# Performance work log

Measured on AMD Instinct MI355X. Metric: run time of the kernel, lower is better.

The kernel has to match this reference:

```python
import jax, jax.numpy as jnp
import numpy as np
import math


def _conv1x1(x, w):
    # x: [B,C,H,W], w: [O,I,1,1] (OIHW)
    return jax.lax.conv_general_dilated(x, w, (1, 1), 'VALID',
                                        dimension_numbers=('NCHW', 'OIHW', 'NCHW'))


def _dwconv3x3(x, w):
    # depthwise 3x3, padding=1; w: [C,1,3,3]
    return jax.lax.conv_general_dilated(x, w, (1, 1), 'SAME',
                                        dimension_numbers=('NCHW', 'OIHW', 'NCHW'),
                                        feature_group_count=x.shape[1])


def setup_inputs() -> dict:
    key = jax.random.key(0)
    ks = jax.random.split(key, 8)
    B, H, W, C = 4, 1024, 1024, 3
    s = 0.3
    return {
        'x': jax.random.normal(ks[0], (B, H * W, C), dtype=jnp.float32),
        'fhigh': jax.random.normal(ks[1], (B, 3, H, W), dtype=jnp.float32),
        'q_C_w': jax.random.normal(ks[2], (3, 3, 1, 1), dtype=jnp.float32) * s,
        'q_dw_w': jax.random.normal(ks[3], (3, 1, 3, 3), dtype=jnp.float32) * s,
        'kv_C_w': jax.random.normal(ks[4], (3, 3, 1, 1), dtype=jnp.float32) * s,
        'kv_dw_w': jax.random.normal(ks[5], (3, 1, 3, 3), dtype=jnp.float32) * s,
        'proj_w': jax.random.normal(ks[6], (3, 3, 1, 1), dtype=jnp.float32) * s,
        'proj_b': jax.random.normal(ks[7], (3,), dtype=jnp.float32) * s,
        'temperature': jnp.ones((1, 1, 1), dtype=jnp.float32),  # num_heads=1
    }


def _l2norm(t):
    # torch F.normalize(dim=-1, eps=1e-12)
    n = jnp.linalg.norm(t, axis=-1, keepdims=True)
    return t / jnp.maximum(n, 1e-12)


def reference(x, fhigh, q_C_w, q_dw_w, kv_C_w, kv_dw_w, proj_w, proj_b, temperature):
    B, N, C = x.shape
    hh = int(math.sqrt(N))
    num_heads = temperature.shape[0]
    # b (h w) c -> b c h w
    xi = x.transpose(0, 2, 1).reshape(B, C, hh, hh)
    q = _dwconv3x3(_conv1x1(fhigh, q_C_w), q_dw_w)     # [B,3,hh,hh]
    kv = _dwconv3x3(_conv1x1(xi, kv_C_w), kv_dw_w)     # [B,C,hh,hh] (k_c == v_c in source)
    # b (head c) h w -> b head c (h w)
    q = q.reshape(B, num_heads, q.shape[1] // num_heads, hh * hh)
    k = kv.reshape(B, num_heads, C // num_heads, hh * hh)
    v = k
    attn = jnp.einsum('bhcn,bhdn->bhcd', _l2norm(q), _l2norm(k)) * temperature  # [B,H,cq,ck]
    attn = jax.nn.softmax(attn, axis=-1)
    x2 = jnp.einsum('bhcd,bhdn->bhcn', attn, v)         # [B,H,cq,N]
    x2 = x2.reshape(B, -1, hh, hh)                       # b (head c) h w
    x2 = _conv1x1(x2, proj_w) + proj_b[None, :, None, None]
    # b c h w -> b (h w) c
    return x2.reshape(B, C, N).transpose(0, 2, 1)
```

## Files before the change

kernel.cpp:

```cpp
#include <hip/hip_runtime.h>

#define H 1024
#define W 1024
#define NPIX (H*W)
#define BATCH 4
#define TX 64
#define TY 16
#define HX 66
#define HXP 68
#define HY 18
#define NHALO (HY*HX)
#define NT 4
#define SLOTS 32
#define PART_FLOATS (BATCH*15*SLOTS)

__global__ __launch_bounds__(256) void pass1(
    const float* __restrict__ x, const float* __restrict__ fhigh,
    const float* __restrict__ qCw, const float* __restrict__ qdw,
    const float* __restrict__ kCw, const float* __restrict__ kdw,
    float* __restrict__ partials)
{
  __shared__ alignas(16) float qm[3][HY][HXP];
  __shared__ alignas(16) float km[3][HY][HXP];
  __shared__ float rb[4][15];

  const int tid = threadIdx.x;
  const int tileX = blockIdx.x;
  const int tileY4 = blockIdx.y;
  const int b = blockIdx.z;

  float wqc[9], wkc[9], wqd[27], wkd[27];
  #pragma unroll
  for (int i = 0; i < 9; i++) { wqc[i] = qCw[i]; wkc[i] = kCw[i]; }
  #pragma unroll
  for (int i = 0; i < 27; i++) { wqd[i] = qdw[i]; wkd[i] = kdw[i]; }

  const float* fb = fhigh + (size_t)b * 3 * NPIX;
  const float* xb = x + (size_t)b * NPIX * 3;

  const int tx = tid & 15;
  const int ty = tid >> 4;

  float acc[15];
  #pragma unroll
  for (int i = 0; i < 15; i++) acc[i] = 0.f;

  for (int t = 0; t < NT; ++t) {
    const int row0 = (tileY4 * NT + t) * TY;

    __syncthreads();
    for (int l = tid; l < NHALO; l += 256) {
      int hy = l / HX;
      int hx = l - hy * HX;
      int gy = row0 + hy - 1;
      int gx = tileX * TX + hx - 1;
      float f0 = 0.f, f1 = 0.f, f2 = 0.f, x0 = 0.f, x1 = 0.f, x2 = 0.f;
      if ((unsigned)gy < H && (unsigned)gx < W) {
        int p = gy * W + gx;
        f0 = fb[p]; f1 = fb[NPIX + p]; f2 = fb[2 * NPIX + p];
        const float* xp = xb + (size_t)p * 3;
        x0 = xp[0]; x1 = xp[1]; x2 = xp[2];
      }
      qm[0][hy][hx] = wqc[0]*f0 + wqc[1]*f1 + wqc[2]*f2;
      qm[1][hy][hx] = wqc[3]*f0 + wqc[4]*f1 + wqc[5]*f2;
      qm[2][hy][hx] = wqc[6]*f0 + wqc[7]*f1 + wqc[8]*f2;
      km[0][hy][hx] = wkc[0]*x0 + wkc[1]*x1 + wkc[2]*x2;
      km[1][hy][hx] = wkc[3]*x0 + wkc[4]*x1 + wkc[5]*x2;
      km[2][hy][hx] = wkc[6]*x0 + wkc[7]*x1 + wkc[8]*x2;
    }
    __syncthreads();

    float qv[3][4], kv[3][4];
    #pragma unroll
    for (int c = 0; c < 3; ++c) {
      #pragma unroll
      for (int i = 0; i < 4; ++i) { qv[c][i] = 0.f; kv[c][i] = 0.f; }
      #pragma unroll
      for (int dy = 0; dy < 3; ++dy) {
        const float4 a0 = *(const float4*)&qm[c][ty + dy][4 * tx];
        const float4 a1 = *(const float4*)&qm[c][ty + dy][4 * tx + 4];
        const float b0 = *(const float*)0 == *(const float*)0 ? 0.f : 0.f; (void)b0;
        const float q0 = wqd[c*9 + dy*3 + 0], q1 = wqd[c*9 + dy*3 + 1], q2 = wqd[c*9 + dy*3 + 2];
        qv[c][0] += q0*a0.x + q1*a0.y + q2*a0.z;
        qv[c][1] += q0*a0.y + q1*a0.z + q2*a0.w;
        qv[c][2] += q0*a0.z + q1*a0.w + q2*a1.x;
        qv[c][3] += q0*a0.w + q1*a1.x + q2*a1.y;
        const float4 c0v = *(const float4*)&km[c][ty + dy][4 * tx];
        const float4 c1v = *(const float4*)&km[c][ty + dy][4 * tx + 4];
        const float k0 = wkd[c*9 + dy*3 + 0], k1 = wkd[c*9 + dy*3 + 1], k2 = wkd[c*9 + dy*3 + 2];
        kv[c][0] += k0*c0v.x + k1*c0v.y + k2*c0v.z;
        kv[c][1] += k0*c0v.y + k1*c0v.z + k2*c0v.w;
        kv[c][2] += k0*c0v.z + k1*c0v.w + k2*c1v.x;
        kv[c][3] += k0*c0v.w + k1*c1v.x + k2*c1v.y;
      }
    }
    #pragma unroll
    for (int i = 0; i < 4; ++i) {
      #pragma unroll
      for (int c = 0; c < 3; ++c) { acc[c] += qv[c][i]*qv[c][i]; acc[3+c] += kv[c][i]*kv[c][i]; }
      #pragma unroll
      for (int c = 0; c < 3; ++c)
        #pragma unroll
        for (int d = 0; d < 3; ++d) acc[6 + c*3 + d] += qv[c][i]*kv[d][i];
    }
  }

  #pragma unroll
  for (int off = 32; off >= 1; off >>= 1)
    #pragma unroll
    for (int i = 0; i < 15; i++)
      acc[i] += __shfl_down(acc[i], off, 64);

  const int wave = tid >> 6;
  if ((tid & 63) == 0) {
    #pragma unroll
    for (int i = 0; i < 15; i++) rb[wave][i] = acc[i];
  }
  __syncthreads();
  if (tid < 15) {
    float s = rb[0][tid] + rb[1][tid] + rb[2][tid] + rb[3][tid];
    int slot = (blockIdx.y * 16 + blockIdx.x) & (SLOTS - 1);
    atomicAdd(&partials[((b * 15 + tid) * SLOTS) + slot], s);
  }
}

__global__ void pass2(const float* __restrict__ partials,
                      const float* __restrict__ proj_w,
                      const float* __restrict__ temperature,
                      float* __restrict__ M)
{
  int b = threadIdx.x;
  if (b >= BATCH) return;
  float sums[15];
  #pragma unroll
  for (int i = 0; i < 15; i++) {
    float s = 0.f;
    for (int sl = 0; sl < SLOTS; sl++) s += partials[((b * 15 + i) * SLOTS) + sl];
    sums[i] = s;
  }
  float qn[3], kn[3];
  #pragma unroll
  for (int c = 0; c < 3; c++) { qn[c] = sqrtf(sums[c]); kn[c] = sqrtf(sums[3 + c]); }
  float t = temperature[0];
  float attn[3][3];
  #pragma unroll
  for (int c = 0; c < 3; c++) {
    float l[3];
    #pragma unroll
    for (int d = 0; d < 3; d++)
      l[d] = sums[6 + c*3 + d] / fmaxf(qn[c], 1e-12f) / fmaxf(kn[d], 1e-12f) * t;
    float m = fmaxf(l[0], fmaxf(l[1], l[2]));
    float e0 = expf(l[0] - m), e1 = expf(l[1] - m), e2 = expf(l[2] - m);
    float inv = 1.f / (e0 + e1 + e2);
    attn[c][0] = e0 * inv; attn[c][1] = e1 * inv; attn[c][2] = e2 * inv;
  }
  #pragma unroll
  for (int c = 0; c < 3; c++)
    #pragma unroll
    for (int d = 0; d < 3; d++)
      M[b * 9 + c * 3 + d] = proj_w[c*3+0]*attn[0][d]
                           + proj_w[c*3+1]*attn[1][d]
                           + proj_w[c*3+2]*attn[2][d];
}

__global__ __launch_bounds__(256) void pass3(
    const float* __restrict__ x,
    const float* __restrict__ kCw, const float* __restrict__ kdw,
    const float* __restrict__ M, const float* __restrict__ proj_b,
    float* __restrict__ out)
{
  __shared__ alignas(16) float km[3][HY][HXP];

  const int tid = threadIdx.x;
  const int tileX = blockIdx.x;
  const int tileY = blockIdx.y;
  const int b = blockIdx.z;

  float wkc[9], wkd[27];
  #pragma unroll
  for (int i = 0; i < 9; i++) wkc[i] = kCw[i];
  #pragma unroll
  for (int i = 0; i < 27; i++) wkd[i] = kdw[i];
  float m[9];
  #pragma unroll
  for (int i = 0; i < 9; i++) m[i] = M[b * 9 + i];
  float pb[3];
  #pragma unroll
  for (int c = 0; c < 3; c++) pb[c] = proj_b[c];

  const float* xb = x + (size_t)b * NPIX * 3;
  const int row0 = tileY * TY;

  for (int l = tid; l < NHALO; l += 256) {
    int hy = l / HX;
    int hx = l - hy * HX;
    int gy = row0 + hy - 1;
    int gx = tileX * TX + hx - 1;
    float x0 = 0.f, x1 = 0.f, x2 = 0.f;
    if ((unsigned)gy < H && (unsigned)gx < W) {
      const float* xp = xb + (size_t)(gy * W + gx) * 3;
      x0 = xp[0]; x1 = xp[1]; x2 = xp[2];
    }
    km[0][hy][hx] = wkc[0]*x0 + wkc[1]*x1 + wkc[2]*x2;
    km[1][hy][hx] = wkc[3]*x0 + wkc[4]*x1 + wkc[5]*x2;
    km[2][hy][hx] = wkc[6]*x0 + wkc[7]*x1 + wkc[8]*x2;
  }
  __syncthreads();

  const int tx = tid & 15;
  const int ty = tid >> 4;

  float kv[3][4];
  #pragma unroll
  for (int c = 0; c < 3; ++c) {
    #pragma unroll
    for (int i = 0; i < 4; ++i) kv[c][i] = 0.f;
    #pragma unroll
    for (int dy = 0; dy < 3; ++dy) {
      const float4 c0v = *(const float4*)&km[c][ty + dy][4 * tx];
      const float4 c1v = *(const float4*)&km[c][ty + dy][4 * tx + 4];
      const float k0 = wkd[c*9 + dy*3 + 0], k1 = wkd[c*9 + dy*3 + 1], k2 = wkd[c*9 + dy*3 + 2];
      kv[c][0] += k0*c0v.x + k1*c0v.y + k2*c0v.z;
      kv[c][1] += k0*c0v.y + k1*c0v.z + k2*c0v.w;
      kv[c][2] += k0*c0v.z + k1*c0v.w + k2*c1v.x;
      kv[c][3] += k0*c0v.w + k1*c1v.x + k2*c1v.y;
    }
  }

  float o[4][3];
  #pragma unroll
  for (int i = 0; i < 4; ++i) {
    #pragma unroll
    for (int oc = 0; oc < 3; ++oc)
      o[i][oc] = m[oc*3+0]*kv[0][i] + m[oc*3+1]*kv[1][i] + m[oc*3+2]*kv[2][i] + pb[oc];
  }

  const int p0 = (row0 + ty) * W + tileX * TX + 4 * tx;
  float* op = out + ((size_t)b * NPIX + p0) * 3;
  float4 w0, w1, w2;
  w0.x = o[0][0]; w0.y = o[0][1]; w0.z = o[0][2]; w0.w = o[1][0];
  w1.x = o[1][1]; w1.y = o[1][2]; w1.z = o[2][0]; w1.w = o[2][1];
  w2.x = o[2][2]; w2.y = o[3][0]; w2.z = o[3][1]; w2.w = o[3][2];
  *(float4*)(op)     = w0;
  *(float4*)(op + 4) = w1;
  *(float4*)(op + 8) = w2;
}

extern "C" void kernel_launch(void* const* d_in, const int* in_sizes, int n_in,
                              void* d_out, int out_size, void* d_ws, size_t ws_size,
                              hipStream_t stream) {
  const float* x     = (const float*)d_in[0];
  const float* fhigh = (const float*)d_in[1];
  const float* qCw   = (const float*)d_in[2];
  const float* qdw   = (const float*)d_in[3];
  const float* kCw   = (const float*)d_in[4];
  const float* kdw   = (const float*)d_in[5];
  const float* pw    = (const float*)d_in[6];
  const float* pb    = (const float*)d_in[7];
  const float* temp  = (const float*)d_in[8];
  float* out = (float*)d_out;

  float* partials = (float*)d_ws;
  float* M = partials + PART_FLOATS;

  hipMemsetAsync(partials, 0, PART_FLOATS * sizeof(float), stream);

  dim3 grid1(W / TX, H / (TY * NT), BATCH);
  pass1<<<grid1, 256, 0, stream>>>(x, fhigh, qCw, qdw, kCw, kdw, partials);
  pass2<<<1, 64, 0, stream>>>(partials, pw, temp, M);
  dim3 grid3(W / TX, H / TY, BATCH);
  pass3<<<grid3, 256, 0, stream>>>(x, kCw, kdw, M, pb, out);
}
```

Before: 203.3 us.

## Replace LDS halo tiles with single-wave register row streaming and shuffles

Both passes now run as 64-thread single-wave blocks, each covering a 256-column by 4-row strip. Rows are loaded with vector loads directly into registers through a rolling three-row buffer, and horizontal neighbours are exchanged with wave shuffles instead of going through shared memory. This removes LDS traffic, __syncthreads and the redundant halo loads. The small pass2 kernel is dropped: every pass3 block recomputes the 3x3 attention/projection matrix from the partials, saving one launch at the cost of redundant partial reads. In exchange, vertical halo reuse drops (6 loaded rows per 4 output rows) and occupancy depends on the much smaller blocks.

```diff
diff --git a/kernel.cpp b/kernel.cpp
--- a/kernel.cpp
+++ b/kernel.cpp
@@ -4,246 +4,320 @@
 #define W 1024
 #define NPIX (H*W)
 #define BATCH 4
-#define TX 64
-#define TY 16
-#define HX 66
-#define HXP 68
-#define HY 18
-#define NHALO (HY*HX)
-#define NT 4
+#define SH 4
 #define SLOTS 32
 #define PART_FLOATS (BATCH*15*SLOTS)
 
-__global__ __launch_bounds__(256) void pass1(
+struct Raw {
+  float4 X0, X1, X2;
+  float4 F0, F1, F2;
+  float4 XE;
+  float  FE0, FE1, FE2;
+};
+
+struct RawX {
+  float4 X0, X1, X2, XE;
+};
+
+__global__ __launch_bounds__(64) void pass1(
     const float* __restrict__ x, const float* __restrict__ fhigh,
     const float* __restrict__ qCw, const float* __restrict__ qdw,
     const float* __restrict__ kCw, const float* __restrict__ kdw,
     float* __restrict__ partials)
 {
-  __shared__ alignas(16) float qm[3][HY][HXP];
-  __shared__ alignas(16) float km[3][HY][HXP];
-  __shared__ float rb[4][15];
-
-  const int tid = threadIdx.x;
-  const int tileX = blockIdx.x;
-  const int tileY4 = blockIdx.y;
-  const int b = blockIdx.z;
+  const int l  = threadIdx.x;
+  const int bx = blockIdx.x;
+  const int b  = blockIdx.y;
+  const int seg = bx & 3;
+  const int r0  = (bx >> 2) * SH;
+  const int c0  = seg * 256 + l * 4;
+  const bool eL = (l == 0)  && (c0 > 0);
+  const bool eR = (l == 63) && (c0 + 4 < W);
 
   float wqc[9], wkc[9], wqd[27], wkd[27];
   #pragma unroll
-  for (int i = 0; i < 9; i++) { wqc[i] = qCw[i]; wkc[i] = kCw[i]; }
+  for (int i = 0; i < 9; i++)  { wqc[i] = qCw[i]; wkc[i] = kCw[i]; }
   #pragma unroll
   for (int i = 0; i < 27; i++) { wqd[i] = qdw[i]; wkd[i] = kdw[i]; }
 
+  const float* xb = x     + (size_t)b * NPIX * 3;
   const float* fb = fhigh + (size_t)b * 3 * NPIX;
-  const float* xb = x + (size_t)b * NPIX * 3;
-
-  const int tx = tid & 15;
-  const int ty = tid >> 4;
-
+
+  float qmid[3][3][4], kmid[3][3][4];
+  float qe[3][3], ke[3][3];
   float acc[15];
   #pragma unroll
   for (int i = 0; i < 15; i++) acc[i] = 0.f;
 
-  for (int t = 0; t < NT; ++t) {
-    const int row0 = (tileY4 * NT + t) * TY;
-
-    __syncthreads();
-    for (int l = tid; l < NHALO; l += 256) {
-      int hy = l / HX;
-      int hx = l - hy * HX;
-      int gy = row0 + hy - 1;
-      int gx = tileX * TX + hx - 1;
-      float f0 = 0.f, f1 = 0.f, f2 = 0.f, x0 = 0.f, x1 = 0.f, x2 = 0.f;
-      if ((unsigned)gy < H && (unsigned)gx < W) {
-        int p = gy * W + gx;
-        f0 = fb[p]; f1 = fb[NPIX + p]; f2 = fb[2 * NPIX + p];
-        const float* xp = xb + (size_t)p * 3;
-        x0 = xp[0]; x1 = xp[1]; x2 = xp[2];
+  Raw A, B2;
+
+  auto LOAD = [&](Raw& S, int r) {
+    const float4 z4 = {0.f, 0.f, 0.f, 0.f};
+    S.X0 = z4; S.X1 = z4; S.X2 = z4; S.F0 = z4; S.F1 = z4; S.F2 = z4; S.XE = z4;
+    S.FE0 = 0.f; S.FE1 = 0.f; S.FE2 = 0.f;
+    if ((unsigned)r < (unsigned)H) {
+      const float* xr = xb + (size_t)r * (W * 3);
+      const float* fr = fb + (size_t)r * W;
+      S.X0 = *(const float4*)(xr + c0 * 3);
+      S.X1 = *(const float4*)(xr + c0 * 3 + 4);
+      S.X2 = *(const float4*)(xr + c0 * 3 + 8);
+      S.F0 = *(const float4*)(fr + c0);
+      S.F1 = *(const float4*)(fr + NPIX + c0);
+      S.F2 = *(const float4*)(fr + 2 * NPIX + c0);
+      if (eL) {
+        S.XE  = *(const float4*)(xr + (c0 - 4) * 3 + 8);
+        S.FE0 = fr[c0 - 1]; S.FE1 = fr[NPIX + c0 - 1]; S.FE2 = fr[2 * NPIX + c0 - 1];
+      } else if (eR) {
+        S.XE  = *(const float4*)(xr + (c0 + 4) * 3);
+        S.FE0 = fr[c0 + 4]; S.FE1 = fr[NPIX + c0 + 4]; S.FE2 = fr[2 * NPIX + c0 + 4];
       }
-      qm[0][hy][hx] = wqc[0]*f0 + wqc[1]*f1 + wqc[2]*f2;
-      qm[1][hy][hx] = wqc[3]*f0 + wqc[4]*f1 + wqc[5]*f2;
-      qm[2][hy][hx] = wqc[6]*f0 + wqc[7]*f1 + wqc[8]*f2;
-      km[0][hy][hx] = wkc[0]*x0 + wkc[1]*x1 + wkc[2]*x2;
-      km[1][hy][hx] = wkc[3]*x0 + wkc[4]*x1 + wkc[5]*x2;
-      km[2][hy][hx] = wkc[6]*x0 + wkc[7]*x1 + wkc[8]*x2;
-    }
-    __syncthreads();
-
+    }
+  };
+
+  auto MID = [&](const Raw& S, int P) {
+    float xc0[4] = {S.X0.x, S.X0.w, S.X1.z, S.X2.y};
+    float xc1[4] = {S.X0.y, S.X1.x, S.X1.w, S.X2.z};
+    float xc2[4] = {S.X0.z, S.X1.y, S.X2.x, S.X2.w};
+    float fc0[4] = {S.F0.x, S.F0.y, S.F0.z, S.F0.w};
+    float fc1[4] = {S.F1.x, S.F1.y, S.F1.z, S.F1.w};
+    float fc2[4] = {S.F2.x, S.F2.y, S.F2.z, S.F2.w};
+    #pragma unroll
+    for (int c = 0; c < 3; c++) {
+      #pragma unroll
+      for (int i = 0; i < 4; i++) {
+        kmid[P][c][i] = wkc[c*3+0]*xc0[i] + wkc[c*3+1]*xc1[i] + wkc[c*3+2]*xc2[i];
+        qmid[P][c][i] = wqc[c*3+0]*fc0[i] + wqc[c*3+1]*fc1[i] + wqc[c*3+2]*fc2[i];
+      }
+    }
+    float ex0 = eL ? S.XE.y : S.XE.x;
+    float ex1 = eL ? S.XE.z : S.XE.y;
+    float ex2 = eL ? S.XE.w : S.XE.z;
+    #pragma unroll
+    for (int c = 0; c < 3; c++) {
+      ke[P][c] = wkc[c*3+0]*ex0 + wkc[c*3+1]*ex1 + wkc[c*3+2]*ex2;
+      qe[P][c] = wqc[c*3+0]*S.FE0 + wqc[c*3+1]*S.FE1 + wqc[c*3+2]*S.FE2;
+    }
+  };
+
+  auto CONS = [&](int j) {
     float qv[3][4], kv[3][4];
     #pragma unroll
-    for (int c = 0; c < 3; ++c) {
-      #pragma unroll
-      for (int i = 0; i < 4; ++i) { qv[c][i] = 0.f; kv[c][i] = 0.f; }
-      #pragma unroll
-      for (int dy = 0; dy < 3; ++dy) {
-        const float4 a0 = *(const float4*)&qm[c][ty + dy][4 * tx];
-        const float4 a1 = *(const float4*)&qm[c][ty + dy][4 * tx + 4];
-        const float b0 = *(const float*)0 == *(const float*)0 ? 0.f : 0.f; (void)b0;
-        const float q0 = wqd[c*9 + dy*3 + 0], q1 = wqd[c*9 + dy*3 + 1], q2 = wqd[c*9 + dy*3 + 2];
-        qv[c][0] += q0*a0.x + q1*a0.y + q2*a0.z;
-        qv[c][1] += q0*a0.y + q1*a0.z + q2*a0.w;
-        qv[c][2] += q0*a0.z + q1*a0.w + q2*a1.x;
-        qv[c][3] += q0*a0.w + q1*a1.x + q2*a1.y;
-        const float4 c0v = *(const float4*)&km[c][ty + dy][4 * tx];
-        const float4 c1v = *(const float4*)&km[c][ty + dy][4 * tx + 4];
-        const float k0 = wkd[c*9 + dy*3 + 0], k1 = wkd[c*9 + dy*3 + 1], k2 = wkd[c*9 + dy*3 + 2];
-        kv[c][0] += k0*c0v.x + k1*c0v.y + k2*c0v.z;
-        kv[c][1] += k0*c0v.y + k1*c0v.z + k2*c0v.w;
-        kv[c][2] += k0*c0v.z + k1*c0v.w + k2*c1v.x;
-        kv[c][3] += k0*c0v.w + k1*c1v.x + k2*c1v.y;
+    for (int c = 0; c < 3; c++)
+      #pragma unroll
+      for (int i = 0; i < 4; i++) { qv[c][i] = 0.f; kv[c][i] = 0.f; }
+    #pragma unroll
+    for (int dy = 0; dy < 3; dy++) {
+      const int P = (j + dy) % 3;
+      #pragma unroll
+      for (int c = 0; c < 3; c++) {
+        {
+          float m0 = qmid[P][c][0], m1 = qmid[P][c][1], m2 = qmid[P][c][2], m3 = qmid[P][c][3];
+          float ml = __shfl_up(m3, 1, 64);   ml = (l == 0)  ? qe[P][c] : ml;
+          float mr = __shfl_down(m0, 1, 64); mr = (l == 63) ? qe[P][c] : mr;
+          float w0 = wqd[c*9+dy*3+0], w1 = wqd[c*9+dy*3+1], w2 = wqd[c*9+dy*3+2];
+          qv[c][0] += w0*ml + w1*m0 + w2*m1;
+          qv[c][1] += w0*m0 + w1*m1 + w2*m2;
+          qv[c][2] += w0*m1 + w1*m2 + w2*m3;
+          qv[c][3] += w0*m2 + w1*m3 + w2*mr;
+        }
+        {
+          float m0 = kmid[P][c][0], m1 = kmid[P][c][1], m2 = kmid[P][c][2], m3 = kmid[P][c][3];
+          float ml = __shfl_up(m3, 1, 64);   ml = (l == 0)  ? ke[P][c] : ml;
+          float mr = __shfl_down(m0, 1, 64); mr = (l == 63) ? ke[P][c] : mr;
+          float w0 = wkd[c*9+dy*3+0], w1 = wkd[c*9+dy*3+1], w2 = wkd[c*9+dy*3+2];
+          kv[c][0] += w0*ml + w1*m0 + w2*m1;
+          kv[c][1] += w0*m0 + w1*m1 + w2*m2;
+          kv[c][2] += w0*m1 + w1*m2 + w2*m3;
+          kv[c][3] += w0*m2 + w1*m3 + w2*mr;
+        }
       }
     }
     #pragma unroll
-    for (int i = 0; i < 4; ++i) {
-      #pragma unroll
-      for (int c = 0; c < 3; ++c) { acc[c] += qv[c][i]*qv[c][i]; acc[3+c] += kv[c][i]*kv[c][i]; }
-      #pragma unroll
-      for (int c = 0; c < 3; ++c)
+    for (int i = 0; i < 4; i++) {
+      #pragma unroll
+      for (int c = 0; c < 3; c++) { acc[c] += qv[c][i]*qv[c][i]; acc[3+c] += kv[c][i]*kv[c][i]; }
+      #pragma unroll
+      for (int c = 0; c < 3; c++)
         #pragma unroll
-        for (int d = 0; d < 3; ++d) acc[6 + c*3 + d] += qv[c][i]*kv[d][i];
-    }
-  }
+        for (int d = 0; d < 3; d++) acc[6 + c*3 + d] += qv[c][i]*kv[d][i];
+    }
+  };
+
+  LOAD(A,  r0 - 1);
+  LOAD(B2, r0);
+  MID(A, 0);
+  LOAD(A,  r0 + 1);
+  MID(B2, 1);
+  LOAD(B2, r0 + 2);
+  MID(A, 2);
+  CONS(0);
+  LOAD(A,  r0 + 3);
+  MID(B2, 0);
+  CONS(1);
+  LOAD(B2, r0 + 4);
+  MID(A, 1);
+  CONS(2);
+  MID(B2, 2);
+  CONS(3);
 
   #pragma unroll
   for (int off = 32; off >= 1; off >>= 1)
     #pragma unroll
     for (int i = 0; i < 15; i++)
-      acc[i] += __shfl_down(acc[i], off, 64);
-
-  const int wave = tid >> 6;
-  if ((tid & 63) == 0) {
-    #pragma unroll
-    for (int i = 0; i < 15; i++) rb[wave][i] = acc[i];
-  }
-  __syncthreads();
-  if (tid < 15) {
-    float s = rb[0][tid] + rb[1][tid] + rb[2][tid] + rb[3][tid];
-    int slot = (blockIdx.y * 16 + blockIdx.x) & (SLOTS - 1);
-    atomicAdd(&partials[((b * 15 + tid) * SLOTS) + slot], s);
+      acc[i] += __shfl_xor(acc[i], off, 64);
+
+  if (l == 0) {
+    const int slot = bx & (SLOTS - 1);
+    #pragma unroll
+    for (int i = 0; i < 15; i++)
+      atomicAdd(&partials[(b * 15 + i) * SLOTS + slot], acc[i]);
   }
 }
 
-__global__ void pass2(const float* __restrict__ partials,
-                      const float* __restrict__ proj_w,
-                      const float* __restrict__ temperature,
-                      float* __restrict__ M)
+__global__ __launch_bounds__(64) void pass3(
+    const float* __restrict__ x,
+    const float* __restrict__ kCw, const float* __restrict__ kdw,
+    const float* __restrict__ partials,
+    const float* __restrict__ proj_w, const float* __restrict__ proj_b,
+    const float* __restrict__ temperature,
+    float* __restrict__ out)
 {
-  int b = threadIdx.x;
-  if (b >= BATCH) return;
+  const int l  = threadIdx.x;
+  const int bx = blockIdx.x;
+  const int b  = blockIdx.y;
+  const int seg = bx & 3;
+  const int r0  = (bx >> 2) * SH;
+  const int c0  = seg * 256 + l * 4;
+  const bool eL = (l == 0)  && (c0 > 0);
+  const bool eR = (l == 63) && (c0 + 4 < W);
+
   float sums[15];
   #pragma unroll
   for (int i = 0; i < 15; i++) {
     float s = 0.f;
-    for (int sl = 0; sl < SLOTS; sl++) s += partials[((b * 15 + i) * SLOTS) + sl];
+    #pragma unroll 8
+    for (int sl = 0; sl < SLOTS; sl++) s += partials[(b * 15 + i) * SLOTS + sl];
     sums[i] = s;
   }
   float qn[3], kn[3];
   #pragma unroll
   for (int c = 0; c < 3; c++) { qn[c] = sqrtf(sums[c]); kn[c] = sqrtf(sums[3 + c]); }
-  float t = temperature[0];
+  const float t = temperature[0];
   float attn[3][3];
   #pragma unroll
   for (int c = 0; c < 3; c++) {
-    float l[3];
+    float lg[3];
     #pragma unroll
     for (int d = 0; d < 3; d++)
-      l[d] = sums[6 + c*3 + d] / fmaxf(qn[c], 1e-12f) / fmaxf(kn[d], 1e-12f) * t;
-    float m = fmaxf(l[0], fmaxf(l[1], l[2]));
-    float e0 = expf(l[0] - m), e1 = expf(l[1] - m), e2 = expf(l[2] - m);
+      lg[d] = sums[6 + c*3 + d] / fmaxf(qn[c], 1e-12f) / fmaxf(kn[d], 1e-12f) * t;
+    float mx = fmaxf(lg[0], fmaxf(lg[1], lg[2]));
+    float e0 = expf(lg[0] - mx), e1 = expf(lg[1] - mx), e2 = expf(lg[2] - mx);
     float inv = 1.f / (e0 + e1 + e2);
     attn[c][0] = e0 * inv; attn[c][1] = e1 * inv; attn[c][2] = e2 * inv;
   }
-  #pragma unroll
-  for (int c = 0; c < 3; c++)
+  float m[3][3];
+  #pragma unroll
+  for (int o = 0; o < 3; o++)
     #pragma unroll
     for (int d = 0; d < 3; d++)
-      M[b * 9 + c * 3 + d] = proj_w[c*3+0]*attn[0][d]
-                           + proj_w[c*3+1]*attn[1][d]
-                           + proj_w[c*3+2]*attn[2][d];
-}
-
-__global__ __launch_bounds__(256) void pass3(
-    const float* __restrict__ x,
-    const float* __restrict__ kCw, const float* __restrict__ kdw,
-    const float* __restrict__ M, const float* __restrict__ proj_b,
-    float* __restrict__ out)
-{
-  __shared__ alignas(16) float km[3][HY][HXP];
-
-  const int tid = threadIdx.x;
-  const int tileX = blockIdx.x;
-  const int tileY = blockIdx.y;
-  const int b = blockIdx.z;
+      m[o][d] = proj_w[o*3+0]*attn[0][d] + proj_w[o*3+1]*attn[1][d] + proj_w[o*3+2]*attn[2][d];
+  float pb[3] = {proj_b[0], proj_b[1], proj_b[2]};
 
   float wkc[9], wkd[27];
   #pragma unroll
-  for (int i = 0; i < 9; i++) wkc[i] = kCw[i];
+  for (int i = 0; i < 9; i++)  wkc[i] = kCw[i];
   #pragma unroll
   for (int i = 0; i < 27; i++) wkd[i] = kdw[i];
-  float m[9];
-  #pragma unroll
-  for (int i = 0; i < 9; i++) m[i] = M[b * 9 + i];
-  float pb[3];
-  #pragma unroll
-  for (int c = 0; c < 3; c++) pb[c] = proj_b[c];
 
   const float* xb = x + (size_t)b * NPIX * 3;
-  const int row0 = tileY * TY;
-
-  for (int l = tid; l < NHALO; l += 256) {
-    int hy = l / HX;
-    int hx = l - hy * HX;
-    int gy = row0 + hy - 1;
-    int gx = tileX * TX + hx - 1;
-    float x0 = 0.f, x1 = 0.f, x2 = 0.f;
-    if ((unsigned)gy < H && (unsigned)gx < W) {
-      const float* xp = xb + (size_t)(gy * W + gx) * 3;
-      x0 = xp[0]; x1 = xp[1]; x2 = xp[2];
-    }
-    km[0][hy][hx] = wkc[0]*x0 + wkc[1]*x1 + wkc[2]*x2;
-    km[1][hy][hx] = wkc[3]*x0 + wkc[4]*x1 + wkc[5]*x2;
-    km[2][hy][hx] = wkc[6]*x0 + wkc[7]*x1 + wkc[8]*x2;
-  }
-  __syncthreads();
-
-  const int tx = tid & 15;
-  const int ty = tid >> 4;
-
-  float kv[3][4];
-  #pragma unroll
-  for (int c = 0; c < 3; ++c) {
-    #pragma unroll
-    for (int i = 0; i < 4; ++i) kv[c][i] = 0.f;
-    #pragma unroll
-    for (int dy = 0; dy < 3; ++dy) {
-      const float4 c0v = *(const float4*)&km[c][ty + dy][4 * tx];
-      const float4 c1v = *(const float4*)&km[c][ty + dy][4 * tx + 4];
-      const float k0 = wkd[c*9 + dy*3 + 0], k1 = wkd[c*9 + dy*3 + 1], k2 = wkd[c*9 + dy*3 + 2];
-      kv[c][0] += k0*c0v.x + k1*c0v.y + k2*c0v.z;
-      kv[c][1] += k0*c0v.y + k1*c0v.z + k2*c0v.w;
-      kv[c][2] += k0*c0v.z + k1*c0v.w + k2*c1v.x;
-      kv[c][3] += k0*c0v.w + k1*c1v.x + k2*c1v.y;
-    }
-  }
-
-  float o[4][3];
-  #pragma unroll
-  for (int i = 0; i < 4; ++i) {
-    #pragma unroll
-    for (int oc = 0; oc < 3; ++oc)
-      o[i][oc] = m[oc*3+0]*kv[0][i] + m[oc*3+1]*kv[1][i] + m[oc*3+2]*kv[2][i] + pb[oc];
-  }
-
-  const int p0 = (row0 + ty) * W + tileX * TX + 4 * tx;
-  float* op = out + ((size_t)b * NPIX + p0) * 3;
-  float4 w0, w1, w2;
-  w0.x = o[0][0]; w0.y = o[0][1]; w0.z = o[0][2]; w0.w = o[1][0];
-  w1.x = o[1][1]; w1.y = o[1][2]; w1.z = o[2][0]; w1.w = o[2][1];
-  w2.x = o[2][2]; w2.y = o[3][0]; w2.z = o[3][1]; w2.w = o[3][2];
-  *(float4*)(op)     = w0;
-  *(float4*)(op + 4) = w1;
-  *(float4*)(op + 8) = w2;
+  float* ob = out + (size_t)b * NPIX * 3;
+
+  float kmid[3][3][4], ke[3][3];
+  RawX A, B2;
+
+  auto LOAD = [&](RawX& S, int r) {
+    const float4 z4 = {0.f, 0.f, 0.f, 0.f};
+    S.X0 = z4; S.X1 = z4; S.X2 = z4; S.XE = z4;
+    if ((unsigned)r < (unsigned)H) {
+      const float* xr = xb + (size_t)r * (W * 3);
+      S.X0 = *(const float4*)(xr + c0 * 3);
+      S.X1 = *(const float4*)(xr + c0 * 3 + 4);
+      S.X2 = *(const float4*)(xr + c0 * 3 + 8);
+      if (eL)      S.XE = *(const float4*)(xr + (c0 - 4) * 3 + 8);
+      else if (eR) S.XE = *(const float4*)(xr + (c0 + 4) * 3);
+    }
+  };
+
+  auto MID = [&](const RawX& S, int P) {
+    float xc0[4] = {S.X0.x, S.X0.w, S.X1.z, S.X2.y};
+    float xc1[4] = {S.X0.y, S.X1.x, S.X1.w, S.X2.z};
+    float xc2[4] = {S.X0.z, S.X1.y, S.X2.x, S.X2.w};
+    #pragma unroll
+    for (int c = 0; c < 3; c++)
+      #pragma unroll
+      for (int i = 0; i < 4; i++)
+        kmid[P][c][i] = wkc[c*3+0]*xc0[i] + wkc[c*3+1]*xc1[i] + wkc[c*3+2]*xc2[i];
+    float ex0 = eL ? S.XE.y : S.XE.x;
+    float ex1 = eL ? S.XE.z : S.XE.y;
+    float ex2 = eL ? S.XE.w : S.XE.z;
+    #pragma unroll
+    for (int c = 0; c < 3; c++)
+      ke[P][c] = wkc[c*3+0]*ex0 + wkc[c*3+1]*ex1 + wkc[c*3+2]*ex2;
+  };
+
+  auto CONS = [&](int j) {
+    float kv[3][4];
+    #pragma unroll
+    for (int c = 0; c < 3; c++)
+      #pragma unroll
+      for (int i = 0; i < 4; i++) kv[c][i] = 0.f;
+    #pragma unroll
+    for (int dy = 0; dy < 3; dy++) {
+      const int P = (j + dy) % 3;
+      #pragma unroll
+      for (int c = 0; c < 3; c++) {
+        float m0 = kmid[P][c][0], m1 = kmid[P][c][1], m2 = kmid[P][c][2], m3 = kmid[P][c][3];
+        float ml = __shfl_up(m3, 1, 64);   ml = (l == 0)  ? ke[P][c] : ml;
+        float mr = __shfl_down(m0, 1, 64); mr = (l == 63) ? ke[P][c] : mr;
+        float w0 = wkd[c*9+dy*3+0], w1 = wkd[c*9+dy*3+1], w2 = wkd[c*9+dy*3+2];
+        kv[c][0] += w0*ml + w1*m0 + w2*m1;
+        kv[c][1] += w0*m0 + w1*m1 + w2*m2;
+        kv[c][2] += w0*m1 + w1*m2 + w2*m3;
+        kv[c][3] += w0*m2 + w1*m3 + w2*mr;
+      }
+    }
+    float o[4][3];
+    #pragma unroll
+    for (int i = 0; i < 4; i++)
+      #pragma unroll
+      for (int oc = 0; oc < 3; oc++)
+        o[i][oc] = m[oc][0]*kv[0][i] + m[oc][1]*kv[1][i] + m[oc][2]*kv[2][i] + pb[oc];
+    float* orow = ob + ((size_t)(r0 + j) * W + c0) * 3;
+    float4 w0, w1, w2;
+    w0.x = o[0][0]; w0.y = o[0][1]; w0.z = o[0][2]; w0.w = o[1][0];
+    w1.x = o[1][1]; w1.y = o[1][2]; w1.z = o[2][0]; w1.w = o[2][1];
+    w2.x = o[2][2]; w2.y = o[3][0]; w2.z = o[3][1]; w2.w = o[3][2];
+    *(float4*)(orow)     = w0;
+    *(float4*)(orow + 4) = w1;
+    *(float4*)(orow + 8) = w2;
+  };
+
+  LOAD(A,  r0 - 1);
+  LOAD(B2, r0);
+  MID(A, 0);
+  LOAD(A,  r0 + 1);
+  MID(B2, 1);
+  LOAD(B2, r0 + 2);
+  MID(A, 2);
+  CONS(0);
+  LOAD(A,  r0 + 3);
+  MID(B2, 0);
+  CONS(1);
+  LOAD(B2, r0 + 4);
+  MID(A, 1);
+  CONS(2);
+  MID(B2, 2);
+  CONS(3);
 }
 
 extern "C" void kernel_launch(void* const* d_in, const int* in_sizes, int n_in,
@@ -261,13 +335,9 @@
   float* out = (float*)d_out;
 
   float* partials = (float*)d_ws;
-  float* M = partials + PART_FLOATS;
-
   hipMemsetAsync(partials, 0, PART_FLOATS * sizeof(float), stream);
 
-  dim3 grid1(W / TX, H / (TY * NT), BATCH);
-  pass1<<<grid1, 256, 0, stream>>>(x, fhigh, qCw, qdw, kCw, kdw, partials);
-  pass2<<<1, 64, 0, stream>>>(partials, pw, temp, M);
-  dim3 grid3(W / TX, H / TY, BATCH);
-  pass3<<<grid3, 256, 0, stream>>>(x, kCw, kdw, M, pb, out);
+  dim3 grid(4 * (H / SH), BATCH);
+  pass1<<<grid, 64, 0, stream>>>(x, fhigh, qCw, qdw, kCw, kdw, partials);
+  pass3<<<grid, 64, 0, stream>>>(x, kCw, kdw, partials, pw, pb, temp, out);
 }
```

Measured after the change: 220.4 us. 1.08x slower.

## Fuse attention-matrix computation into output pass and restructure halo loads

Applied to the files above, without the earlier changes.

Removes the single-thread pass2 kernel. Every pass3 block now reduces the partial sums itself and computes the softmax and projection matrix, which saves one launch and its serialization. Halo loading switches to one wave per row with float4 loads of x, and q/k are interleaved in one shared buffer. Pass3 also now processes four row tiles per block. The cost is redundant per-block reduction work in pass3 (15×32 global reads per thread) and fewer, larger pass3 blocks.

```diff
diff --git a/kernel.cpp b/kernel.cpp
--- a/kernel.cpp
+++ b/kernel.cpp
@@ -4,15 +4,13 @@
 #define W 1024
 #define NPIX (H*W)
 #define BATCH 4
-#define TX 64
-#define TY 16
-#define HX 66
-#define HXP 68
-#define HY 18
-#define NHALO (HY*HX)
+#define TW 64
+#define TH 16
 #define NT 4
 #define SLOTS 32
 #define PART_FLOATS (BATCH*15*SLOTS)
+#define R1 140
+#define R3 68
 
 __global__ __launch_bounds__(256) void pass1(
     const float* __restrict__ x, const float* __restrict__ fhigh,
@@ -20,88 +18,99 @@
     const float* __restrict__ kCw, const float* __restrict__ kdw,
     float* __restrict__ partials)
 {
-  __shared__ alignas(16) float qm[3][HY][HXP];
-  __shared__ alignas(16) float km[3][HY][HXP];
+  __shared__ alignas(16) float m[3 * 18 * R1];
   __shared__ float rb[4][15];
 
   const int tid = threadIdx.x;
-  const int tileX = blockIdx.x;
-  const int tileY4 = blockIdx.y;
-  const int b = blockIdx.z;
+  const int wv = tid >> 6, ln = tid & 63;
+  const int tx = tid & 15, ty = tid >> 4;
+  const int tileX = blockIdx.x, tY = blockIdx.y, b = blockIdx.z;
+  const int cx0 = tileX * TW;
 
   float wqc[9], wkc[9], wqd[27], wkd[27];
   #pragma unroll
-  for (int i = 0; i < 9; i++) { wqc[i] = qCw[i]; wkc[i] = kCw[i]; }
+  for (int i = 0; i < 9; i++)  { wqc[i] = qCw[i]; wkc[i] = kCw[i]; }
   #pragma unroll
   for (int i = 0; i < 27; i++) { wqd[i] = qdw[i]; wkd[i] = kdw[i]; }
 
   const float* fb = fhigh + (size_t)b * 3 * NPIX;
   const float* xb = x + (size_t)b * NPIX * 3;
 
-  const int tx = tid & 15;
-  const int ty = tid >> 4;
-
   float acc[15];
   #pragma unroll
   for (int i = 0; i < 15; i++) acc[i] = 0.f;
 
   for (int t = 0; t < NT; ++t) {
-    const int row0 = (tileY4 * NT + t) * TY;
-
-    __syncthreads();
-    for (int l = tid; l < NHALO; l += 256) {
-      int hy = l / HX;
-      int hx = l - hy * HX;
-      int gy = row0 + hy - 1;
-      int gx = tileX * TX + hx - 1;
-      float f0 = 0.f, f1 = 0.f, f2 = 0.f, x0 = 0.f, x1 = 0.f, x2 = 0.f;
-      if ((unsigned)gy < H && (unsigned)gx < W) {
-        int p = gy * W + gx;
-        f0 = fb[p]; f1 = fb[NPIX + p]; f2 = fb[2 * NPIX + p];
-        const float* xp = xb + (size_t)p * 3;
-        x0 = xp[0]; x1 = xp[1]; x2 = xp[2];
-      }
-      qm[0][hy][hx] = wqc[0]*f0 + wqc[1]*f1 + wqc[2]*f2;
-      qm[1][hy][hx] = wqc[3]*f0 + wqc[4]*f1 + wqc[5]*f2;
-      qm[2][hy][hx] = wqc[6]*f0 + wqc[7]*f1 + wqc[8]*f2;
-      km[0][hy][hx] = wkc[0]*x0 + wkc[1]*x1 + wkc[2]*x2;
-      km[1][hy][hx] = wkc[3]*x0 + wkc[4]*x1 + wkc[5]*x2;
-      km[2][hy][hx] = wkc[6]*x0 + wkc[7]*x1 + wkc[8]*x2;
+    const int row0 = (tY * NT + t) * TH;
+    __syncthreads();
+
+    #pragma unroll
+    for (int kk = 0; kk < 5; ++kk) {
+      const int hy = wv + 4 * kk;
+      if (hy < 18) {
+        const int gy = row0 - 1 + hy;
+        const bool rv = (unsigned)gy < (unsigned)H;
+        #pragma unroll
+        for (int e = 0; e < 2; ++e) {
+          if (e == 0 || ln < 2) {
+            const int hx = e ? (64 + ln) : ln;
+            const int gx = cx0 - 1 + hx;
+            float f0=0.f,f1=0.f,f2=0.f,x0=0.f,x1=0.f,x2=0.f;
+            if (rv && (unsigned)gx < (unsigned)W) {
+              const float* fr = fb + (size_t)gy * W + gx;
+              f0 = fr[0]; f1 = fr[NPIX]; f2 = fr[2*NPIX];
+              const float* xr = xb + ((size_t)gy * W + gx) * 3;
+              if (gx < W - 1) { float4 v = *(const float4*)xr; x0=v.x; x1=v.y; x2=v.z; }
+              else            { x0 = xr[0]; x1 = xr[1]; x2 = xr[2]; }
+            }
+            #pragma unroll
+            for (int c = 0; c < 3; c++) {
+              float2 p;
+              p.x = wqc[c*3+0]*f0 + wqc[c*3+1]*f1 + wqc[c*3+2]*f2;
+              p.y = wkc[c*3+0]*x0 + wkc[c*3+1]*x1 + wkc[c*3+2]*x2;
+              *(float2*)&m[(c*18 + hy)*R1 + 2*hx] = p;
+            }
+          }
+        }
+      }
     }
     __syncthreads();
 
     float qv[3][4], kv[3][4];
     #pragma unroll
-    for (int c = 0; c < 3; ++c) {
-      #pragma unroll
-      for (int i = 0; i < 4; ++i) { qv[c][i] = 0.f; kv[c][i] = 0.f; }
-      #pragma unroll
-      for (int dy = 0; dy < 3; ++dy) {
-        const float4 a0 = *(const float4*)&qm[c][ty + dy][4 * tx];
-        const float4 a1 = *(const float4*)&qm[c][ty + dy][4 * tx + 4];
-        const float b0 = *(const float*)0 == *(const float*)0 ? 0.f : 0.f; (void)b0;
-        const float q0 = wqd[c*9 + dy*3 + 0], q1 = wqd[c*9 + dy*3 + 1], q2 = wqd[c*9 + dy*3 + 2];
-        qv[c][0] += q0*a0.x + q1*a0.y + q2*a0.z;
-        qv[c][1] += q0*a0.y + q1*a0.z + q2*a0.w;
-        qv[c][2] += q0*a0.z + q1*a0.w + q2*a1.x;
-        qv[c][3] += q0*a0.w + q1*a1.x + q2*a1.y;
-        const float4 c0v = *(const float4*)&km[c][ty + dy][4 * tx];
-        const float4 c1v = *(const float4*)&km[c][ty + dy][4 * tx + 4];
-        const float k0 = wkd[c*9 + dy*3 + 0], k1 = wkd[c*9 + dy*3 + 1], k2 = wkd[c*9 + dy*3 + 2];
-        kv[c][0] += k0*c0v.x + k1*c0v.y + k2*c0v.z;
-        kv[c][1] += k0*c0v.y + k1*c0v.z + k2*c0v.w;
-        kv[c][2] += k0*c0v.z + k1*c0v.w + k2*c1v.x;
-        kv[c][3] += k0*c0v.w + k1*c1v.x + k2*c1v.y;
-      }
-    }
-    #pragma unroll
-    for (int i = 0; i < 4; ++i) {
-      #pragma unroll
-      for (int c = 0; c < 3; ++c) { acc[c] += qv[c][i]*qv[c][i]; acc[3+c] += kv[c][i]*kv[c][i]; }
-      #pragma unroll
-      for (int c = 0; c < 3; ++c)
+    for (int c = 0; c < 3; c++)
+      #pragma unroll
+      for (int i = 0; i < 4; i++) { qv[c][i] = 0.f; kv[c][i] = 0.f; }
+
+    #pragma unroll
+    for (int dy = 0; dy < 3; dy++) {
+      const int hy = ty + dy;
+      #pragma unroll
+      for (int c = 0; c < 3; c++) {
+        const float* mr = &m[(c*18 + hy)*R1 + 8*tx];
+        const float4 A  = *(const float4*)(mr);
+        const float4 Bv = *(const float4*)(mr + 4);
+        const float4 Cv = *(const float4*)(mr + 8);
+        const float a0=wqd[c*9+dy*3+0], a1=wqd[c*9+dy*3+1], a2=wqd[c*9+dy*3+2];
+        qv[c][0] += a0*A.x  + a1*A.z  + a2*Bv.x;
+        qv[c][1] += a0*A.z  + a1*Bv.x + a2*Bv.z;
+        qv[c][2] += a0*Bv.x + a1*Bv.z + a2*Cv.x;
+        qv[c][3] += a0*Bv.z + a1*Cv.x + a2*Cv.z;
+        const float b0=wkd[c*9+dy*3+0], b1=wkd[c*9+dy*3+1], b2=wkd[c*9+dy*3+2];
+        kv[c][0] += b0*A.y  + b1*A.w  + b2*Bv.y;
+        kv[c][1] += b0*A.w  + b1*Bv.y + b2*Bv.w;
+        kv[c][2] += b0*Bv.y + b1*Bv.w + b2*Cv.y;
+        kv[c][3] += b0*Bv.w + b1*Cv.y + b2*Cv.w;
+      }
+    }
+    #pragma unroll
+    for (int i = 0; i < 4; i++) {
+      #pragma unroll
+      for (int c = 0; c < 3; c++) { acc[c] += qv[c][i]*qv[c][i]; acc[3+c] += kv[c][i]*kv[c][i]; }
+      #pragma unroll
+      for (int c = 0; c < 3; c++)
         #pragma unroll
-        for (int d = 0; d < 3; ++d) acc[6 + c*3 + d] += qv[c][i]*kv[d][i];
+        for (int d = 0; d < 3; d++) acc[6 + c*3 + d] += qv[c][i]*kv[d][i];
     }
   }
 
@@ -109,141 +118,145 @@
   for (int off = 32; off >= 1; off >>= 1)
     #pragma unroll
     for (int i = 0; i < 15; i++)
-      acc[i] += __shfl_down(acc[i], off, 64);
-
-  const int wave = tid >> 6;
-  if ((tid & 63) == 0) {
-    #pragma unroll
-    for (int i = 0; i < 15; i++) rb[wave][i] = acc[i];
+      acc[i] += __shfl_xor(acc[i], off, 64);
+
+  if (ln == 0) {
+    #pragma unroll
+    for (int i = 0; i < 15; i++) rb[wv][i] = acc[i];
   }
   __syncthreads();
   if (tid < 15) {
     float s = rb[0][tid] + rb[1][tid] + rb[2][tid] + rb[3][tid];
-    int slot = (blockIdx.y * 16 + blockIdx.x) & (SLOTS - 1);
-    atomicAdd(&partials[((b * 15 + tid) * SLOTS) + slot], s);
-  }
-}
-
-__global__ void pass2(const float* __restrict__ partials,
-                      const float* __restrict__ proj_w,
-                      const float* __restrict__ temperature,
-                      float* __restrict__ M)
-{
-  int b = threadIdx.x;
-  if (b >= BATCH) return;
-  float sums[15];
-  #pragma unroll
-  for (int i = 0; i < 15; i++) {
-    float s = 0.f;
-    for (int sl = 0; sl < SLOTS; sl++) s += partials[((b * 15 + i) * SLOTS) + sl];
-    sums[i] = s;
-  }
-  float qn[3], kn[3];
-  #pragma unroll
-  for (int c = 0; c < 3; c++) { qn[c] = sqrtf(sums[c]); kn[c] = sqrtf(sums[3 + c]); }
-  float t = temperature[0];
-  float attn[3][3];
-  #pragma unroll
-  for (int c = 0; c < 3; c++) {
-    float l[3];
-    #pragma unroll
-    for (int d = 0; d < 3; d++)
-      l[d] = sums[6 + c*3 + d] / fmaxf(qn[c], 1e-12f) / fmaxf(kn[d], 1e-12f) * t;
-    float m = fmaxf(l[0], fmaxf(l[1], l[2]));
-    float e0 = expf(l[0] - m), e1 = expf(l[1] - m), e2 = expf(l[2] - m);
-    float inv = 1.f / (e0 + e1 + e2);
-    attn[c][0] = e0 * inv; attn[c][1] = e1 * inv; attn[c][2] = e2 * inv;
-  }
-  #pragma unroll
-  for (int c = 0; c < 3; c++)
-    #pragma unroll
-    for (int d = 0; d < 3; d++)
-      M[b * 9 + c * 3 + d] = proj_w[c*3+0]*attn[0][d]
-                           + proj_w[c*3+1]*attn[1][d]
-                           + proj_w[c*3+2]*attn[2][d];
+    const int slot = (tY * 16 + tileX) & (SLOTS - 1);
+    atomicAdd(&partials[(b * 15 + tid) * SLOTS + slot], s);
+  }
 }
 
 __global__ __launch_bounds__(256) void pass3(
     const float* __restrict__ x,
     const float* __restrict__ kCw, const float* __restrict__ kdw,
-    const float* __restrict__ M, const float* __restrict__ proj_b,
+    const float* __restrict__ partials,
+    const float* __restrict__ proj_w, const float* __restrict__ proj_b,
+    const float* __restrict__ temperature,
     float* __restrict__ out)
 {
-  __shared__ alignas(16) float km[3][HY][HXP];
+  __shared__ alignas(16) float mk[3 * 18 * R3];
 
   const int tid = threadIdx.x;
-  const int tileX = blockIdx.x;
-  const int tileY = blockIdx.y;
-  const int b = blockIdx.z;
+  const int wv = tid >> 6, ln = tid & 63;
+  const int tx = tid & 15, ty = tid >> 4;
+  const int tileX = blockIdx.x, tY = blockIdx.y, b = blockIdx.z;
+  const int cx0 = tileX * TW;
+
+  float sums[15];
+  #pragma unroll
+  for (int i = 0; i < 15; i++) {
+    float s = 0.f;
+    #pragma unroll 8
+    for (int sl = 0; sl < SLOTS; sl++) s += partials[(b * 15 + i) * SLOTS + sl];
+    sums[i] = s;
+  }
+  float qn[3], kn[3];
+  #pragma unroll
+  for (int c = 0; c < 3; c++) { qn[c] = sqrtf(sums[c]); kn[c] = sqrtf(sums[3 + c]); }
+  const float tmp = temperature[0];
+  float attn[3][3];
+  #pragma unroll
+  for (int c = 0; c < 3; c++) {
+    float lg[3];
+    #pragma unroll
+    for (int d = 0; d < 3; d++)
+      lg[d] = sums[6 + c*3 + d] / fmaxf(qn[c], 1e-12f) / fmaxf(kn[d], 1e-12f) * tmp;
+    float mx = fmaxf(lg[0], fmaxf(lg[1], lg[2]));
+    float e0 = expf(lg[0]-mx), e1 = expf(lg[1]-mx), e2 = expf(lg[2]-mx);
+    float inv = 1.f / (e0 + e1 + e2);
+    attn[c][0] = e0*inv; attn[c][1] = e1*inv; attn[c][2] = e2*inv;
+  }
+  float M[3][3];
+  #pragma unroll
+  for (int o = 0; o < 3; o++)
+    #pragma unroll
+    for (int d = 0; d < 3; d++)
+      M[o][d] = proj_w[o*3+0]*attn[0][d] + proj_w[o*3+1]*attn[1][d] + proj_w[o*3+2]*attn[2][d];
+  const float pb0 = proj_b[0], pb1 = proj_b[1], pb2 = proj_b[2];
 
   float wkc[9], wkd[27];
   #pragma unroll
-  for (int i = 0; i < 9; i++) wkc[i] = kCw[i];
+  for (int i = 0; i < 9; i++)  wkc[i] = kCw[i];
   #pragma unroll
   for (int i = 0; i < 27; i++) wkd[i] = kdw[i];
-  float m[9];
-  #pragma unroll
-  for (int i = 0; i < 9; i++) m[i] = M[b * 9 + i];
-  float pb[3];
-  #pragma unroll
-  for (int c = 0; c < 3; c++) pb[c] = proj_b[c];
 
   const float* xb = x + (size_t)b * NPIX * 3;
-  const int row0 = tileY * TY;
-
-  for (int l = tid; l < NHALO; l += 256) {
-    int hy = l / HX;
-    int hx = l - hy * HX;
-    int gy = row0 + hy - 1;
-    int gx = tileX * TX + hx - 1;
-    float x0 = 0.f, x1 = 0.f, x2 = 0.f;
-    if ((unsigned)gy < H && (unsigned)gx < W) {
-      const float* xp = xb + (size_t)(gy * W + gx) * 3;
-      x0 = xp[0]; x1 = xp[1]; x2 = xp[2];
-    }
-    km[0][hy][hx] = wkc[0]*x0 + wkc[1]*x1 + wkc[2]*x2;
-    km[1][hy][hx] = wkc[3]*x0 + wkc[4]*x1 + wkc[5]*x2;
-    km[2][hy][hx] = wkc[6]*x0 + wkc[7]*x1 + wkc[8]*x2;
-  }
-  __syncthreads();
-
-  const int tx = tid & 15;
-  const int ty = tid >> 4;
-
-  float kv[3][4];
-  #pragma unroll
-  for (int c = 0; c < 3; ++c) {
-    #pragma unroll
-    for (int i = 0; i < 4; ++i) kv[c][i] = 0.f;
-    #pragma unroll
-    for (int dy = 0; dy < 3; ++dy) {
-      const float4 c0v = *(const float4*)&km[c][ty + dy][4 * tx];
-      const float4 c1v = *(const float4*)&km[c][ty + dy][4 * tx + 4];
-      const float k0 = wkd[c*9 + dy*3 + 0], k1 = wkd[c*9 + dy*3 + 1], k2 = wkd[c*9 + dy*3 + 2];
-      kv[c][0] += k0*c0v.x + k1*c0v.y + k2*c0v.z;
-      kv[c][1] += k0*c0v.y + k1*c0v.z + k2*c0v.w;
-      kv[c][2] += k0*c0v.z + k1*c0v.w + k2*c1v.x;
-      kv[c][3] += k0*c0v.w + k1*c1v.x + k2*c1v.y;
-    }
-  }
-
-  float o[4][3];
-  #pragma unroll
-  for (int i = 0; i < 4; ++i) {
-    #pragma unroll
-    for (int oc = 0; oc < 3; ++oc)
-      o[i][oc] = m[oc*3+0]*kv[0][i] + m[oc*3+1]*kv[1][i] + m[oc*3+2]*kv[2][i] + pb[oc];
-  }
-
-  const int p0 = (row0 + ty) * W + tileX * TX + 4 * tx;
-  float* op = out + ((size_t)b * NPIX + p0) * 3;
-  float4 w0, w1, w2;
-  w0.x = o[0][0]; w0.y = o[0][1]; w0.z = o[0][2]; w0.w = o[1][0];
-  w1.x = o[1][1]; w1.y = o[1][2]; w1.z = o[2][0]; w1.w = o[2][1];
-  w2.x = o[2][2]; w2.y = o[3][0]; w2.z = o[3][1]; w2.w = o[3][2];
-  *(float4*)(op)     = w0;
-  *(float4*)(op + 4) = w1;
-  *(float4*)(op + 8) = w2;
+  float* ob = out + (size_t)b * NPIX * 3;
+
+  for (int t = 0; t < NT; ++t) {
+    const int row0 = (tY * NT + t) * TH;
+    __syncthreads();
+
+    #pragma unroll
+    for (int kk = 0; kk < 5; ++kk) {
+      const int hy = wv + 4 * kk;
+      if (hy < 18) {
+        const int gy = row0 - 1 + hy;
+        const bool rv = (unsigned)gy < (unsigned)H;
+        #pragma unroll
+        for (int e = 0; e < 2; ++e) {
+          if (e == 0 || ln < 2) {
+            const int hx = e ? (64 + ln) : ln;
+            const int gx = cx0 - 1 + hx;
+            float x0=0.f,x1=0.f,x2=0.f;
+            if (rv && (unsigned)gx < (unsigned)W) {
+              const float* xr = xb + ((size_t)gy * W + gx) * 3;
+              if (gx < W - 1) { float4 v = *(const float4*)xr; x0=v.x; x1=v.y; x2=v.z; }
+              else            { x0 = xr[0]; x1 = xr[1]; x2 = xr[2]; }
+            }
+            #pragma unroll
+            for (int c = 0; c < 3; c++)
+              mk[(c*18 + hy)*R3 + hx] = wkc[c*3+0]*x0 + wkc[c*3+1]*x1 + wkc[c*3+2]*x2;
+          }
+        }
+      }
+    }
+    __syncthreads();
+
+    float kv[3][4];
+    #pragma unroll
+    for (int c = 0; c < 3; c++)
+      #pragma unroll
+      for (int i = 0; i < 4; i++) kv[c][i] = 0.f;
+
+    #pragma unroll
+    for (int dy = 0; dy < 3; dy++) {
+      const int hy = ty + dy;
+      #pragma unroll
+      for (int c = 0; c < 3; c++) {
+        const float* mr = &mk[(c*18 + hy)*R3 + 4*tx];
+        const float4 A  = *(const float4*)(mr);
+        const float4 Bv = *(const float4*)(mr + 4);
+        const float b0=wkd[c*9+dy*3+0], b1=wkd[c*9+dy*3+1], b2=wkd[c*9+dy*3+2];
+        kv[c][0] += b0*A.x + b1*A.y  + b2*A.z;
+        kv[c][1] += b0*A.y + b1*A.z  + b2*A.w;
+        kv[c][2] += b0*A.z + b1*A.w  + b2*Bv.x;
+        kv[c][3] += b0*A.w + b1*Bv.x + b2*Bv.y;
+      }
+    }
+
+    float o[4][3];
+    #pragma unroll
+    for (int i = 0; i < 4; i++) {
+      o[i][0] = M[0][0]*kv[0][i] + M[0][1]*kv[1][i] + M[0][2]*kv[2][i] + pb0;
+      o[i][1] = M[1][0]*kv[0][i] + M[1][1]*kv[1][i] + M[1][2]*kv[2][i] + pb1;
+      o[i][2] = M[2][0]*kv[0][i] + M[2][1]*kv[1][i] + M[2][2]*kv[2][i] + pb2;
+    }
+    float* op = ob + ((size_t)(row0 + ty) * W + cx0 + 4*tx) * 3;
+    float4 w0, w1, w2;
+    w0.x = o[0][0]; w0.y = o[0][1]; w0.z = o[0][2]; w0.w = o[1][0];
+    w1.x = o[1][1]; w1.y = o[1][2]; w1.z = o[2][0]; w1.w = o[2][1];
+    w2.x = o[2][2]; w2.y = o[3][0]; w2.z = o[3][1]; w2.w = o[3][2];
+    *(float4*)(op)     = w0;
+    *(float4*)(op + 4) = w1;
+    *(float4*)(op + 8) = w2;
+  }
 }
 
 extern "C" void kernel_launch(void* const* d_in, const int* in_sizes, int n_in,
@@ -261,13 +274,9 @@
   float* out = (float*)d_out;
 
   float* partials = (float*)d_ws;
-  float* M = partials + PART_FLOATS;
-
   hipMemsetAsync(partials, 0, PART_FLOATS * sizeof(float), stream);
 
-  dim3 grid1(W / TX, H / (TY * NT), BATCH);
-  pass1<<<grid1, 256, 0, stream>>>(x, fhigh, qCw, qdw, kCw, kdw, partials);
-  pass2<<<1, 64, 0, stream>>>(partials, pw, temp, M);
-  dim3 grid3(W / TX, H / TY, BATCH);
-  pass3<<<grid3, 256, 0, stream>>>(x, kCw, kdw, M, pb, out);
+  dim3 grid(W / TW, H / (TH * NT), BATCH);
+  pass1<<<grid, 256, 0, stream>>>(x, fhigh, qCw, qdw, kCw, kdw, partials);
+  pass3<<<grid, 256, 0, stream>>>(x, kCw, kdw, partials, pw, pb, temp, out);
 }
```

New measurement: 223.6 us. 10.0% more time.
